# Kernel tuning notes

Hardware: AMD Instinct MI355X
Metric: run time of the kernel (lower is better)

Reference implementation:

```python
import jax, jax.numpy as jnp
import numpy as np

B, IN, H, OUT, BS = 2048, 1024, 2048, 1024, 32
RB = H // BS   # 64 block rows of fc2
CB = H // BS   # 64 block cols of fc2
DENSITY = 0.5
K = int(CB * DENSITY)  # 32 nonzero block-cols per block row
NNZ = RB * K           # 2048 nonzero blocks


def setup_inputs() -> dict:
    key = jax.random.key(0)
    k0, k1, k2, k3, k4, k5, k6 = jax.random.split(key, 7)
    # Fixed BSR sparsity structure (constant indices), built with numpy
    rng = np.random.default_rng(0)
    cols = np.stack([np.sort(rng.choice(CB, size=K, replace=False)) for _ in range(RB)])
    col_indices = jnp.asarray(cols.reshape(-1), dtype=jnp.int32)          # [NNZ]
    crow_indices = jnp.asarray(np.arange(RB + 1) * K, dtype=jnp.int32)    # [RB+1]
    s = 0.02
    return {
        "x": jax.random.normal(k0, (B, IN), jnp.float32),
        "W1": jax.random.normal(k1, (H, IN), jnp.float32) * s,
        "b1": jax.random.normal(k2, (H,), jnp.float32) * s,
        "crow_indices": crow_indices,
        "col_indices": col_indices,
        "values": jax.random.normal(k3, (NNZ, BS, BS), jnp.float32) * s,  # BSR blocks of fc2.weight [H,H]
        "b2": jax.random.normal(k4, (H,), jnp.float32) * s,
        "W3": jax.random.normal(k5, (OUT, H), jnp.float32) * s,
        "b3": jax.random.normal(k6, (OUT,), jnp.float32) * s,
    }


def bsr_linear(h, crow_indices, col_indices, values, bias):
    # y = h @ W.T + bias, W stored as BSR (block rows = out blocks, block cols = in blocks)
    b = h.shape[0]
    nnz, bs, _ = values.shape
    rb = crow_indices.shape[0] - 1
    hb = h.reshape(b, -1, bs)                      # [B, CB, bs]
    hg = hb[:, col_indices]                        # [B, NNZ, bs] gather input blocks per nnz block
    # contribution of block k (row r, col c): x_block[c] @ values[k].T
    contrib = jnp.einsum("bnj,nij->nbi", hg, values)  # [NNZ, B, bs]
    # block-row id of each nnz block, jit-safe via searchsorted on crow
    row_ids = jnp.searchsorted(crow_indices, jnp.arange(nnz, dtype=crow_indices.dtype), side="right") - 1
    yb = jax.ops.segment_sum(contrib, row_ids, num_segments=rb)  # [RB, B, bs]
    return jnp.transpose(yb, (1, 0, 2)).reshape(b, rb * bs) + bias


def reference(x, W1, b1, crow_indices, col_indices, values, b2, W3, b3):
    x = x.reshape(x.shape[0], -1)                 # Flatten
    h = jax.nn.relu(x @ W1.T + b1)                # fc1 + ReLU
    h = jax.nn.relu(bsr_linear(h, crow_indices, col_indices, values, b2))  # BSR fc2 + ReLU
    return h @ W3.T + b3                          # fc3
```

## Files before the change

kernel.cpp:

```cpp
#include <hip/hip_runtime.h>
#include <hip/hip_bf16.h>


typedef __attribute__((ext_vector_type(8))) short bf16x8;
typedef __attribute__((ext_vector_type(4))) float f32x4;

__device__ __forceinline__ unsigned short f2bf(float f) {
    union { float f; unsigned int u; } c; c.f = f;
    unsigned int u = c.u;
    u += 0x7fffu + ((u >> 16) & 1u);
    return (unsigned short)(u >> 16);
}

__device__ __forceinline__ void async16(const void* g, void* l) {
    __builtin_amdgcn_global_load_lds(
        (const __attribute__((address_space(1))) void*)g,
        (__attribute__((address_space(3))) void*)l,
        16, 0, 0);
}

template<int N>
__device__ __forceinline__ void vm_wait() {
    asm volatile("s_waitcnt vmcnt(%0)" :: "n"(N) : "memory");
}
__device__ __forceinline__ void barrier() {
    asm volatile("" ::: "memory");
    __builtin_amdgcn_s_barrier();
    asm volatile("" ::: "memory");
}

__global__ __launch_bounds__(256) void cvt4(
    const float* __restrict__ x,  const float* __restrict__ w1,
    const float* __restrict__ w3, const float* __restrict__ v,
    unsigned short* __restrict__ xb,  unsigned short* __restrict__ w1b,
    unsigned short* __restrict__ w3b, unsigned short* __restrict__ vb)
{
    const int NE = 1 << 21;
    int e = (blockIdx.x * 256 + threadIdx.x) * 4;
    int a = e >> 21;
    int off = e & (NE - 1);
    const float* src = (a == 0) ? x : (a == 1) ? w1 : (a == 2) ? w3 : v;
    unsigned short* dst = (a == 0) ? xb : (a == 1) ? w1b : (a == 2) ? w3b : vb;
    float4 vv = *reinterpret_cast<const float4*>(src + off);
    ushort4 o;
    o.x = f2bf(vv.x); o.y = f2bf(vv.y); o.z = f2bf(vv.z); o.w = f2bf(vv.w);
    *reinterpret_cast<ushort4*>(dst + off) = o;
}

__global__ __launch_bounds__(256) void combine2(
    const float* __restrict__ p0, const float* __restrict__ p1,
    const float* __restrict__ b3, float* __restrict__ out)
{
    int i = (blockIdx.x * 256 + threadIdx.x) * 4;
    float4 a = *reinterpret_cast<const float4*>(p0 + i);
    float4 b = *reinterpret_cast<const float4*>(p1 + i);
    float4 c = *reinterpret_cast<const float4*>(b3 + (i & 1023));
    float4 o = {a.x + b.x + c.x, a.y + b.y + c.y,
                a.z + b.z + c.z, a.w + b.w + c.w};
    *reinterpret_cast<float4*>(out + i) = o;
}

template<int BM, int BN, int MCL, int RELU, int OUTMODE>
__global__ __launch_bounds__(256) void gemm_bt(
    const unsigned short* __restrict__ A,
    const unsigned short* __restrict__ B,
    const float* __restrict__ bias,
    void* __restrict__ Cout,
    int M, int N, int K, int kbase, int klen)
{
    constexpr int BK = 64;
    constexpr int MR = BM / 32;
    constexpr int NR = BN / 32;
    constexpr int AI = BM / 32;
    constexpr int BI = BN / 32;
    constexpr int LPS = AI + BI;
    __shared__ unsigned short As[2][BM * BK];
    __shared__ unsigned short Bs[2][BN * BK];

    const int t = threadIdx.x;
    const int w = t >> 6;
    const int l = t & 63;

    const int id = blockIdx.x;
    const int xcd = id & 7;
    const int j = id >> 3;
    const int mt = xcd * MCL + (j & (MCL - 1));
    const int nt = j / MCL;
    const int bm = mt * BM;
    const int bn = nt * BN;

    const int wm = (w >> 1) * (BM / 2);
    const int wn = (w & 1) * (BN / 2);

    f32x4 acc[MR][NR];
    #pragma unroll
    for (int i = 0; i < MR; ++i)
        #pragma unroll
        for (int jj = 0; jj < NR; ++jj)
            acc[i][jj] = (f32x4){0.f, 0.f, 0.f, 0.f};

    const int arow = bm + w * (BM / 4) + (l >> 3);
    const int brow = bn + w * (BN / 4) + (l >> 3);
    const int scol = ((l & 7) ^ (l >> 3)) * 8;

    const int fr = l & 15;
    const int kg = l >> 4;
    const int fq = l >> 4;

    auto stage = [&](int buf, int kt) {
        const int k0 = kbase + kt * BK;
        #pragma unroll
        for (int i = 0; i < AI; ++i)
            async16(A + (size_t)(arow + i * 8) * K + k0 + scol,
                    &As[buf][(w * (BM / 4) + i * 8) * BK]);
        #pragma unroll
        for (int i = 0; i < BI; ++i)
            async16(B + (size_t)(brow + i * 8) * K + k0 + scol,
                    &Bs[buf][(w * (BN / 4) + i * 8) * BK]);
    };

    auto compute = [&](int buf) {
        #pragma unroll
        for (int kk = 0; kk < 2; ++kk) {
            const int pc = ((kk * 4 + kg) ^ (fr & 7)) * 8;
            bf16x8 af[MR], bg[NR];
            #pragma unroll
            for (int i = 0; i < MR; ++i)
                af[i] = *reinterpret_cast<const bf16x8*>(
                    &As[buf][(wm + i * 16 + fr) * BK + pc]);
            #pragma unroll
            for (int jj = 0; jj < NR; ++jj)
                bg[jj] = *reinterpret_cast<const bf16x8*>(
                    &Bs[buf][(wn + jj * 16 + fr) * BK + pc]);
            __builtin_amdgcn_s_setprio(1);
            #pragma unroll
            for (int i = 0; i < MR; ++i)
                #pragma unroll
                for (int jj = 0; jj < NR; ++jj)
                    acc[i][jj] = __builtin_amdgcn_mfma_f32_16x16x32_bf16(
                        af[i], bg[jj], acc[i][jj], 0, 0, 0);
            __builtin_amdgcn_s_setprio(0);
        }
    };

    const int nK = klen >> 6;
    stage(0, 0);
    stage(1, 1);
    int cur = 0;
    for (int kt = 0; kt < nK - 1; ++kt) {
        vm_wait<LPS>();
        barrier();
        compute(cur);
        barrier();
        if (kt + 2 < nK) stage(cur, kt + 2);
        cur ^= 1;
    }
    vm_wait<0>();
    barrier();
    compute(cur);

    #pragma unroll
    for (int i = 0; i < MR; ++i) {
        const int row0 = bm + wm + i * 16 + fq * 4;
        #pragma unroll
        for (int jj = 0; jj < NR; ++jj) {
            const int col = bn + wn + jj * 16 + fr;
            const float bv = (OUTMODE == 2) ? 0.f : bias[col];
            #pragma unroll
            for (int v = 0; v < 4; ++v) {
                float r = acc[i][jj][v] + bv;
                if (RELU) r = fmaxf(r, 0.f);
                const size_t off = (size_t)(row0 + v) * N + col;
                if (OUTMODE == 1) ((unsigned short*)Cout)[off] = f2bf(r);
                else              ((float*)Cout)[off] = r;
            }
        }
    }
}

__global__ __launch_bounds__(256) void bsr_layer(
    const unsigned short* __restrict__ h,
    const int* __restrict__ crow,
    const int* __restrict__ cols,
    const unsigned short* __restrict__ vals,
    const float* __restrict__ b2,
    unsigned short* __restrict__ h2)
{
    __shared__ unsigned short Hs[2][128 * 64];
    __shared__ unsigned short Vs[2][32 * 64];
    __shared__ int colsS[64];
    const int t = threadIdx.x;
    const int w = t >> 6;
    const int l = t & 63;

    const int id = blockIdx.x;
    const int xcd = id & 7;
    const int j2 = id >> 3;
    const int bt = xcd * 2 + (j2 & 1);
    const int r  = j2 >> 1;
    const int bm = bt * 128;

    const int s = crow[r];
    const int cnt = crow[r + 1] - s;
    const int wrow = w * 32;

    if (t < cnt) colsS[t] = cols[s + t];

    f32x4 acc[2][2];
    #pragma unroll
    for (int i = 0; i < 2; ++i)
        #pragma unroll
        for (int jj = 0; jj < 2; ++jj)
            acc[i][jj] = (f32x4){0.f, 0.f, 0.f, 0.f};

    const int fr = l & 15;
    const int kg = l >> 4;
    const int lr = l >> 3;
    const int sc = (l & 7) ^ lr;

    auto stage = [&](int buf, int js) {
        const int n0 = s + 2 * js;
        const bool tail = (2 * js + 1 >= cnt);
        const int c0 = colsS[2 * js];
        const int c1 = tail ? c0 : colsS[2 * js + 1];
        const int n1 = tail ? n0 : n0 + 1;
        #pragma unroll
        for (int i = 0; i < 4; ++i) {
            const int row = bm + w * 32 + i * 8 + lr;
            const int col = (sc & 4) ? c1 * 32 + (sc & 3) * 8 : c0 * 32 + sc * 8;
            async16(h + (size_t)row * 2048 + col,
                    &Hs[buf][(w * 32 + i * 8) * 64]);
        }
        const int vrow = w * 8 + lr;
        if (!tail || !(sc & 4)) {
            const unsigned short* src =
                vals + (size_t)((sc & 4) ? n1 : n0) * 1024 + vrow * 32 + (sc & 3) * 8;
            async16(src, &Vs[buf][(w * 8) * 64]);
        } else {
            bf16x8 z = (bf16x8){0,0,0,0,0,0,0,0};
            *reinterpret_cast<bf16x8*>(&Vs[buf][vrow * 64 + (l & 7) * 8]) = z;
        }
    };

    auto compute = [&](int buf) {
        #pragma unroll
        for (int kk = 0; kk < 2; ++kk) {
            const int pc = ((kk * 4 + kg) ^ (fr & 7)) * 8;
            bf16x8 af[2], bg[2];
            #pragma unroll
            for (int i = 0; i < 2; ++i)
                af[i] = *reinterpret_cast<const bf16x8*>(
                    &Hs[buf][(wrow + i * 16 + fr) * 64 + pc]);
            #pragma unroll
            for (int jj = 0; jj < 2; ++jj)
                bg[jj] = *reinterpret_cast<const bf16x8*>(
                    &Vs[buf][(jj * 16 + fr) * 64 + pc]);
            __builtin_amdgcn_s_setprio(1);
            #pragma unroll
            for (int i = 0; i < 2; ++i)
                #pragma unroll
                for (int jj = 0; jj < 2; ++jj)
                    acc[i][jj] = __builtin_amdgcn_mfma_f32_16x16x32_bf16(
                        af[i], bg[jj], acc[i][jj], 0, 0, 0);
            __builtin_amdgcn_s_setprio(0);
        }
    };

    __syncthreads();
    const int nsteps = (cnt + 1) >> 1;
    stage(0, 0);
    if (nsteps > 1) stage(1, 1);
    int cur = 0;
    for (int js = 0; js < nsteps - 1; ++js) {
        vm_wait<5>();
        barrier();
        compute(cur);
        barrier();
        if (js + 2 < nsteps) stage(cur, js + 2);
        cur ^= 1;
    }
    vm_wait<0>();
    barrier();
    compute(cur);

    const int fq = l >> 4;
    #pragma unroll
    for (int i = 0; i < 2; ++i) {
        const int row0 = bm + wrow + i * 16 + fq * 4;
        #pragma unroll
        for (int jj = 0; jj < 2; ++jj) {
            const int col = r * 32 + jj * 16 + fr;
            const float bv = b2[col];
            #pragma unroll
            for (int v = 0; v < 4; ++v) {
                float rv = fmaxf(acc[i][jj][v] + bv, 0.f);
                h2[(size_t)(row0 + v) * 2048 + col] = f2bf(rv);
            }
        }
    }
}

extern "C" void kernel_launch(void* const* d_in, const int* in_sizes, int n_in,
                              void* d_out, int out_size, void* d_ws, size_t ws_size,
                              hipStream_t stream) {
    const float* x    = (const float*)d_in[0];
    const float* W1   = (const float*)d_in[1];
    const float* b1   = (const float*)d_in[2];
    const int*   crow = (const int*)d_in[3];
    const int*   cols = (const int*)d_in[4];
    const float* vals = (const float*)d_in[5];
    const float* b2   = (const float*)d_in[6];
    const float* W3   = (const float*)d_in[7];
    const float* b3   = (const float*)d_in[8];
    float* out = (float*)d_out;

    const int NE = 2 * 1024 * 1024;
    unsigned short* xb  = (unsigned short*)d_ws;
    unsigned short* w1b = xb  + NE;
    unsigned short* w3b = w1b + NE;
    unsigned short* vb  = w3b + NE;
    unsigned short* hb  = vb  + NE;
    unsigned short* h2b = hb  + 2 * NE;
    float* p0 = (float*)d_ws;
    float* p1 = (float*)hb;

    cvt4<<<8192, 256, 0, stream>>>(x, W1, W3, vals, xb, w1b, w3b, vb);

    gemm_bt<64, 64, 4, 1, 1><<<1024, 256, 0, stream>>>(
        xb, w1b, b1, hb, 2048, 2048, 1024, 0, 1024);
    bsr_layer<<<1024, 256, 0, stream>>>(hb, crow, cols, vb, b2, h2b);
    gemm_bt<64, 64, 4, 0, 2><<<512, 256, 0, stream>>>(
        h2b, w3b, nullptr, p0, 2048, 1024, 2048, 0, 1024);
    gemm_bt<64, 64, 4, 0, 2><<<512, 256, 0, stream>>>(
        h2b, w3b, nullptr, p1, 2048, 1024, 2048, 1024, 1024);
    combine2<<<2048, 256, 0, stream>>>(p0, p1, b3, out);

    (void)in_sizes; (void)n_in; (void)out_size; (void)ws_size;
}
```

Before: 87.39 us.

## Add triple-buffer GEMM pipeline, merge split-K launches, retile fc1, drop setprio

```diff
diff --git a/kernel.cpp b/kernel.cpp
--- a/kernel.cpp
+++ b/kernel.cpp
@@ -60,13 +60,14 @@
     *reinterpret_cast<float4*>(out + i) = o;
 }
 
-template<int BM, int BN, int MCL, int RELU, int OUTMODE>
+template<int BM, int BN, int MCL, int KSPLIT, int PIPE, int RELU, int OUTMODE>
 __global__ __launch_bounds__(256) void gemm_bt(
     const unsigned short* __restrict__ A,
     const unsigned short* __restrict__ B,
     const float* __restrict__ bias,
-    void* __restrict__ Cout,
-    int M, int N, int K, int kbase, int klen)
+    void* __restrict__ C0,
+    void* __restrict__ C1,
+    int M, int N, int K)
 {
     constexpr int BK = 64;
     constexpr int MR = BM / 32;
@@ -74,8 +75,8 @@
     constexpr int AI = BM / 32;
     constexpr int BI = BN / 32;
     constexpr int LPS = AI + BI;
-    __shared__ unsigned short As[2][BM * BK];
-    __shared__ unsigned short Bs[2][BN * BK];
+    __shared__ unsigned short As[PIPE][BM * BK];
+    __shared__ unsigned short Bs[PIPE][BN * BK];
 
     const int t = threadIdx.x;
     const int w = t >> 6;
@@ -83,11 +84,14 @@
 
     const int id = blockIdx.x;
     const int xcd = id & 7;
-    const int j = id >> 3;
+    int j = id >> 3;
+    int ks = 0;
+    if (KSPLIT == 2) { ks = j & 1; j >>= 1; }
     const int mt = xcd * MCL + (j & (MCL - 1));
     const int nt = j / MCL;
     const int bm = mt * BM;
     const int bn = nt * BN;
+    const int kb = ks * (K / KSPLIT);
 
     const int wm = (w >> 1) * (BM / 2);
     const int wn = (w & 1) * (BN / 2);
@@ -108,7 +112,7 @@
     const int fq = l >> 4;
 
     auto stage = [&](int buf, int kt) {
-        const int k0 = kbase + kt * BK;
+        const int k0 = kb + kt * BK;
         #pragma unroll
         for (int i = 0; i < AI; ++i)
             async16(A + (size_t)(arow + i * 8) * K + k0 + scol,
@@ -132,32 +136,39 @@
             for (int jj = 0; jj < NR; ++jj)
                 bg[jj] = *reinterpret_cast<const bf16x8*>(
                     &Bs[buf][(wn + jj * 16 + fr) * BK + pc]);
-            __builtin_amdgcn_s_setprio(1);
             #pragma unroll
             for (int i = 0; i < MR; ++i)
                 #pragma unroll
                 for (int jj = 0; jj < NR; ++jj)
                     acc[i][jj] = __builtin_amdgcn_mfma_f32_16x16x32_bf16(
                         af[i], bg[jj], acc[i][jj], 0, 0, 0);
-            __builtin_amdgcn_s_setprio(0);
         }
     };
 
-    const int nK = klen >> 6;
+    const int nK = (K / KSPLIT) >> 6;
     stage(0, 0);
     stage(1, 1);
+    if (PIPE == 3) stage(2, 2);
     int cur = 0;
-    for (int kt = 0; kt < nK - 1; ++kt) {
-        vm_wait<LPS>();
+    for (int kt = 0; kt < nK; ++kt) {
+        if (PIPE == 3) {
+            if (kt < nK - 2)       vm_wait<2 * LPS>();
+            else if (kt == nK - 2) vm_wait<LPS>();
+            else                   vm_wait<0>();
+        } else {
+            if (kt < nK - 1)       vm_wait<LPS>();
+            else                   vm_wait<0>();
+        }
         barrier();
         compute(cur);
-        barrier();
-        if (kt + 2 < nK) stage(cur, kt + 2);
-        cur ^= 1;
+        if (kt + PIPE < nK) {
+            barrier();
+            stage(cur, kt + PIPE);
+        } else if (kt + 1 < nK) {
+            barrier();
+        }
+        cur = (cur == PIPE - 1) ? 0 : cur + 1;
     }
-    vm_wait<0>();
-    barrier();
-    compute(cur);
 
     #pragma unroll
     for (int i = 0; i < MR; ++i) {
@@ -171,8 +182,10 @@
                 float r = acc[i][jj][v] + bv;
                 if (RELU) r = fmaxf(r, 0.f);
                 const size_t off = (size_t)(row0 + v) * N + col;
-                if (OUTMODE == 1) ((unsigned short*)Cout)[off] = f2bf(r);
-                else              ((float*)Cout)[off] = r;
+                if (OUTMODE == 1)
+                    ((unsigned short*)C0)[off] = f2bf(r);
+                else
+                    ((float*)(ks ? C1 : C0))[off] = r;
             }
         }
     }
@@ -255,14 +268,12 @@
             for (int jj = 0; jj < 2; ++jj)
                 bg[jj] = *reinterpret_cast<const bf16x8*>(
                     &Vs[buf][(jj * 16 + fr) * 64 + pc]);
-            __builtin_amdgcn_s_setprio(1);
             #pragma unroll
             for (int i = 0; i < 2; ++i)
                 #pragma unroll
                 for (int jj = 0; jj < 2; ++jj)
                     acc[i][jj] = __builtin_amdgcn_mfma_f32_16x16x32_bf16(
                         af[i], bg[jj], acc[i][jj], 0, 0, 0);
-            __builtin_amdgcn_s_setprio(0);
         }
     };
 
@@ -326,13 +337,11 @@
 
     cvt4<<<8192, 256, 0, stream>>>(x, W1, W3, vals, xb, w1b, w3b, vb);
 
-    gemm_bt<64, 64, 4, 1, 1><<<1024, 256, 0, stream>>>(
-        xb, w1b, b1, hb, 2048, 2048, 1024, 0, 1024);
+    gemm_bt<128, 64, 2, 1, 3, 1, 1><<<512, 256, 0, stream>>>(
+        xb, w1b, b1, hb, nullptr, 2048, 2048, 1024);
     bsr_layer<<<1024, 256, 0, stream>>>(hb, crow, cols, vb, b2, h2b);
-    gemm_bt<64, 64, 4, 0, 2><<<512, 256, 0, stream>>>(
-        h2b, w3b, nullptr, p0, 2048, 1024, 2048, 0, 1024);
-    gemm_bt<64, 64, 4, 0, 2><<<512, 256, 0, stream>>>(
-        h2b, w3b, nullptr, p1, 2048, 1024, 2048, 1024, 1024);
+    gemm_bt<64, 64, 4, 2, 2, 0, 2><<<1024, 256, 0, stream>>>(
+        h2b, w3b, nullptr, p0, p1, 2048, 1024, 2048);
     combine2<<<2048, 256, 0, stream>>>(p0, p1, b3, out);
 
     (void)in_sizes; (void)n_in; (void)out_size; (void)ws_size;
```

Result: faster. 77.82 us (-10.9%).
